# Kernel optimization log

Hardware: AMD Instinct MI355X
Metric: run time of the kernel (lower is better)

## Reference

```python
import jax, jax.numpy as jnp
import numpy as np

V = 100000   # input_size == output_size (item vocab)
H = 256      # hidden_size
B = 512      # batch_size
L = 1        # num_layers


def setup_inputs() -> dict:
    key = jax.random.key(0)
    k0, k1, k2, k3, k4 = jax.random.split(key, 5)
    s = 1.0 / np.sqrt(H)  # pytorch default uniform bound scale
    return {
        "input": jax.random.randint(k0, (B,), 0, V),
        "target": jax.random.randint(k1, (B,), 0, V),
        "hidden": jnp.zeros((L, B, H), jnp.float32),
        # GRU weights, pytorch gate layout [r; z; n]
        "w_ih": jax.random.uniform(k2, (3 * H, V), jnp.float32, -s, s),
        "w_hh": jax.random.uniform(k3, (3 * H, H), jnp.float32, -s, s),
        "b_ih": jnp.zeros((3 * H,), jnp.float32),
        "b_hh": jnp.zeros((3 * H,), jnp.float32),
        # h2o linear
        "w_out": jax.random.uniform(k4, (V, H), jnp.float32, -s, s),
        "b_out": jnp.zeros((V,), jnp.float32),
    }


def reference(input, target, hidden, w_ih, w_hh, b_ih, b_hh, w_out, b_out):
    # one-hot(input) @ w_ih.T is mathematically a column gather of w_ih
    h = hidden[0]                                        # (B, H)
    gi = jnp.take(w_ih, input, axis=1).T + b_ih          # (B, 3H)
    gh = h @ w_hh.T + b_hh                               # (B, 3H)
    i_r, i_z, i_n = jnp.split(gi, 3, axis=1)
    h_r, h_z, h_n = jnp.split(gh, 3, axis=1)
    r = jax.nn.sigmoid(i_r + h_r)
    z = jax.nn.sigmoid(i_z + h_z)
    n = jnp.tanh(i_n + r * h_n)
    h_new = (1.0 - z) * n + z * h                        # (B, H)
    logit = jnp.tanh(h_new @ w_out.T + b_out)            # (B, V)
    return logit, h_new[None]                            # ((B,V), (L,B,H))
```

## Files before the change

kernel.cpp:

```cpp
#include <hip/hip_runtime.h>
#include <hip/hip_bf16.h>
#include <math.h>

#define V 100000
#define H 256
#define B 512

typedef __bf16 bf16x8 __attribute__((ext_vector_type(8)));
typedef unsigned short u16x8 __attribute__((ext_vector_type(8)));
typedef float  f32x4  __attribute__((ext_vector_type(4)));

__device__ __forceinline__ unsigned short f32_bf16_rne(float x) {
    unsigned u = __float_as_uint(x);
    u += 0x7FFFu + ((u >> 16) & 1u);
    return (unsigned short)(u >> 16);
}
__device__ __forceinline__ float bf16u_f32(unsigned short h) {
    return __uint_as_float(((unsigned)h) << 16);
}
__device__ __forceinline__ float fast_tanh(float x) {
    float e = __builtin_exp2f(x * 2.8853900817779268f);
    return 1.f - 2.f * __builtin_amdgcn_rcpf(e + 1.f);
}

#define GLOAD_LDS16(g, l)                                                     \
    __builtin_amdgcn_global_load_lds(                                         \
        (const __attribute__((address_space(1))) void*)(g),                   \
        (__attribute__((address_space(3))) void*)(l), 16, 0, 0)

__global__ __launch_bounds__(256) void gru_cell_v3(
    const int*   __restrict__ input,
    const float* __restrict__ hidden,
    const float* __restrict__ w_ih,
    const float* __restrict__ w_hh,
    const float* __restrict__ b_ih,
    const float* __restrict__ b_hh,
    float*       __restrict__ h_out,
    unsigned short* __restrict__ h_hi_p,
    unsigned short* __restrict__ h_lo_p)
{
    const int gb  = blockIdx.x >> 2;
    const int q   = blockIdx.x & 3;
    const int b0  = gb * 8;
    const int j0  = q * 64;
    const int tid = threadIdx.x;
    const int jj  = tid & 63;
    const int bq  = tid >> 6;
    const int j   = j0 + jj;

    __shared__ float hs[8 * H];
    __shared__ int   idxs[8];
    #pragma unroll
    for (int i = 0; i < 2; ++i) {
        const int p = i * 256 + tid;
        reinterpret_cast<float4*>(hs)[p] =
            reinterpret_cast<const float4*>(hidden + (size_t)b0 * H)[p];
    }
    if (tid < 8) idxs[tid] = input[b0 + tid];
    __syncthreads();

    const int ba = bq * 2, bb = bq * 2 + 1;
    const int ia = idxs[ba], ib = idxs[bb];

    const float g_ra = w_ih[(size_t) j          * V + ia];
    const float g_rb = w_ih[(size_t) j          * V + ib];
    const float g_za = w_ih[(size_t)(j +     H) * V + ia];
    const float g_zb = w_ih[(size_t)(j +     H) * V + ib];
    const float g_na = w_ih[(size_t)(j + 2 * H) * V + ia];
    const float g_nb = w_ih[(size_t)(j + 2 * H) * V + ib];

    const float4* wr = reinterpret_cast<const float4*>(&w_hh[(size_t) j          * H]);
    const float4* wz = reinterpret_cast<const float4*>(&w_hh[(size_t)(j +     H) * H]);
    const float4* wn = reinterpret_cast<const float4*>(&w_hh[(size_t)(j + 2 * H) * H]);
    const float4* ha = reinterpret_cast<const float4*>(&hs[ba * H]);
    const float4* hb = reinterpret_cast<const float4*>(&hs[bb * H]);

    float ara = 0.f, aza = 0.f, ana = 0.f;
    float arb = 0.f, azb = 0.f, anb = 0.f;
    #pragma unroll 4
    for (int k = 0; k < H / 4; ++k) {
        const float4 a = wr[k];
        const float4 c = wz[k];
        const float4 d = wn[k];
        const float4 va = ha[k];
        const float4 vb = hb[k];
        ara += a.x * va.x + a.y * va.y + a.z * va.z + a.w * va.w;
        aza += c.x * va.x + c.y * va.y + c.z * va.z + c.w * va.w;
        ana += d.x * va.x + d.y * va.y + d.z * va.z + d.w * va.w;
        arb += a.x * vb.x + a.y * vb.y + a.z * vb.z + a.w * vb.w;
        azb += c.x * vb.x + c.y * vb.y + c.z * vb.z + c.w * vb.w;
        anb += d.x * vb.x + d.y * vb.y + d.z * vb.z + d.w * vb.w;
    }

    const float bir = b_ih[j], biz = b_ih[j + H], bin = b_ih[j + 2 * H];
    const float bhr = b_hh[j], bhz = b_hh[j + H], bhn = b_hh[j + 2 * H];

    #pragma unroll
    for (int s = 0; s < 2; ++s) {
        const float gi_r = (s ? g_rb : g_ra) + bir;
        const float gi_z = (s ? g_zb : g_za) + biz;
        const float gi_n = (s ? g_nb : g_na) + bin;
        const float h_r  = (s ? arb : ara) + bhr;
        const float h_z  = (s ? azb : aza) + bhz;
        const float h_n  = (s ? anb : ana) + bhn;
        const int   bg   = b0 + (s ? bb : ba);

        const float r = 1.f / (1.f + expf(-(gi_r + h_r)));
        const float z = 1.f / (1.f + expf(-(gi_z + h_z)));
        const float n = tanhf(gi_n + r * h_n);
        const float hprev = hs[(s ? bb : ba) * H + jj + j0];
        const float val = (1.f - z) * n + z * hprev;

        h_out[(size_t)bg * H + j] = val;
        if (h_hi_p != nullptr) {
            const unsigned short hh = f32_bf16_rne(val);
            h_hi_p[(size_t)bg * H + j] = hh;
            h_lo_p[(size_t)bg * H + j] = f32_bf16_rne(val - bf16u_f32(hh));
        }
    }
}

#define DBM  64
#define DBN  256
#define NVB3 391

__global__ __launch_bounds__(256, 2) void out_gemm_direct(
    const float*          __restrict__ w_out,
    const unsigned short* __restrict__ hhi_g,
    const unsigned short* __restrict__ hlo_g,
    const float*          __restrict__ b_out,
    float*                __restrict__ logit)
{
    __shared__ unsigned short h_hi_s[DBM * H];
    __shared__ unsigned short h_lo_s[DBM * H];

    const int tid  = threadIdx.x;
    const int lane = tid & 63;
    const int wid  = tid >> 6;

    const int bid = blockIdx.x;
    const int wg  = (bid & 7) * NVB3 + (bid >> 3);
    const int vb  = wg >> 3;
    const int bx  = wg & 7;
    const int b0  = bx * DBM;
    const int v0  = vb * DBN;
    const int vw  = v0 + wid * 64;

    #pragma unroll
    for (int i = 0; i < 8; ++i) {
        const int pbase = i * 4096 + (wid << 10);
        const int p     = pbase + (lane << 4);
        const int row   = p >> 9;
        const int kb    = p & 511;
        const int swz   = kb ^ ((row & 7) << 4);
        const size_t gb = (size_t)(b0 + row) * 512 + swz;
        GLOAD_LDS16((const char*)hhi_g + gb, (char*)h_hi_s + pbase);
        GLOAD_LDS16((const char*)hlo_g + gb, (char*)h_lo_s + pbase);
    }
    __syncthreads();

    f32x4 acc[4][4];
    #pragma unroll
    for (int m = 0; m < 4; ++m)
        #pragma unroll
        for (int n = 0; n < 4; ++n)
            acc[m][n] = f32x4{0.f, 0.f, 0.f, 0.f};

    auto loadW = [&](float4* wreg, int t) {
        #pragma unroll
        for (int n = 0; n < 4; ++n) {
            int v = vw + n * 16 + (lane & 15);
            if (v > V - 1) v = V - 1;
            const size_t bo = (size_t)v * 1024 + t * 128 + ((lane >> 4) << 5);
            wreg[n * 2]     = *reinterpret_cast<const float4*>(
                                  reinterpret_cast<const char*>(w_out) + bo);
            wreg[n * 2 + 1] = *reinterpret_cast<const float4*>(
                                  reinterpret_cast<const char*>(w_out) + bo + 16);
        }
    };

    auto step = [&](int t, const float4* wreg) {
        const int kbyte = t * 64 + ((lane >> 4) << 4);
        bf16x8 ah[4], al[4];
        #pragma unroll
        for (int m = 0; m < 4; ++m) {
            const int row = m * 16 + (lane & 15);
            const int off = row * 512 + (kbyte ^ ((row & 7) << 4));
            ah[m] = *reinterpret_cast<const bf16x8*>(
                        reinterpret_cast<const char*>(h_hi_s) + off);
            al[m] = *reinterpret_cast<const bf16x8*>(
                        reinterpret_cast<const char*>(h_lo_s) + off);
        }
        bf16x8 bh[4], bl[4];
        #pragma unroll
        for (int n = 0; n < 4; ++n) {
            const float4 fa = wreg[n * 2];
            const float4 fb = wreg[n * 2 + 1];
            const float f[8] = {fa.x, fa.y, fa.z, fa.w, fb.x, fb.y, fb.z, fb.w};
            u16x8 uh, ul;
            #pragma unroll
            for (int e = 0; e < 8; ++e) {
                const unsigned short hv = f32_bf16_rne(f[e]);
                uh[e] = hv;
                ul[e] = f32_bf16_rne(f[e] - bf16u_f32(hv));
            }
            bh[n] = __builtin_bit_cast(bf16x8, uh);
            bl[n] = __builtin_bit_cast(bf16x8, ul);
        }
        #pragma unroll
        for (int n = 0; n < 4; ++n) {
            #pragma unroll
            for (int m = 0; m < 4; ++m) {
                acc[m][n] = __builtin_amdgcn_mfma_f32_16x16x32_bf16(ah[m], bh[n], acc[m][n], 0, 0, 0);
                acc[m][n] = __builtin_amdgcn_mfma_f32_16x16x32_bf16(ah[m], bl[n], acc[m][n], 0, 0, 0);
                acc[m][n] = __builtin_amdgcn_mfma_f32_16x16x32_bf16(al[m], bh[n], acc[m][n], 0, 0, 0);
            }
        }
    };

    float4 wA[8], wB[8];
    loadW(wA, 0);
    #pragma unroll
    for (int tt = 0; tt < 4; ++tt) {
        loadW(wB, tt * 2 + 1);
        step(tt * 2, wA);
        if (tt < 3) loadW(wA, tt * 2 + 2);
        step(tt * 2 + 1, wB);
    }

    float bias[4];
    int   cols[4];
    #pragma unroll
    for (int n = 0; n < 4; ++n) {
        const int c = vw + n * 16 + (lane & 15);
        cols[n] = c;
        bias[n] = (c < V) ? b_out[c] : 0.f;
    }
    const int rbase = b0 + ((lane >> 4) << 2);
    #pragma unroll
    for (int m = 0; m < 4; ++m) {
        #pragma unroll
        for (int r = 0; r < 4; ++r) {
            const int row = rbase + m * 16 + r;
            float* dst = logit + (size_t)row * V;
            #pragma unroll
            for (int n = 0; n < 4; ++n) {
                if (cols[n] < V)
                    dst[cols[n]] = fast_tanh(acc[m][n][r] + bias[n]);
            }
        }
    }
}

#define BM  64
#define BN  128
#define BK  64
#define NVB 782
#define NBB 8

__global__ __launch_bounds__(256) void out_gemm_mfma_reg(
    const float* __restrict__ hnew,
    const float* __restrict__ w_out,
    const float* __restrict__ b_out,
    float*       __restrict__ logit)
{
    __shared__ unsigned short w_hi[BN * BK];
    __shared__ unsigned short w_lo[BN * BK];
    __shared__ unsigned short h_hi[BM * BK];
    __shared__ unsigned short h_lo[BM * BK];

    const int tid  = threadIdx.x;
    const int lane = tid & 63;
    const int wid  = tid >> 6;
    const int wm   = wid >> 1;
    const int wn   = wid & 1;

    const int bid = blockIdx.x;
    const int wg  = (bid & 7) * NVB + (bid >> 3);
    const int bx  = wg & 7;
    const int by  = wg >> 3;
    const int b0  = bx * BM;
    const int v0  = by * BN;

    float4 wreg[8];
    float4 hreg[4];

    auto load_chunk = [&](int k0) {
        #pragma unroll
        for (int i = 0; i < 8; ++i) {
            const int idx4 = i * 256 + tid;
            const int row  = idx4 >> 4;
            const int k4   = (idx4 & 15) << 2;
            int vg = v0 + row; if (vg > V - 1) vg = V - 1;
            wreg[i] = *reinterpret_cast<const float4*>(&w_out[(size_t)vg * H + k0 + k4]);
        }
        #pragma unroll
        for (int i = 0; i < 4; ++i) {
            const int idx4 = i * 256 + tid;
            const int row  = idx4 >> 4;
            const int k4   = (idx4 & 15) << 2;
            hreg[i] = *reinterpret_cast<const float4*>(&hnew[(b0 + row) * H + k0 + k4]);
        }
    };

    auto store_chunk = [&]() {
        #pragma unroll
        for (int i = 0; i < 8; ++i) {
            const int idx4 = i * 256 + tid;
            const int row  = idx4 >> 4;
            const int k4   = (idx4 & 15) << 2;
            const int off  = row * (BK * 2) + ((k4 * 2) ^ ((row & 7) << 4));
            const float f[4] = {wreg[i].x, wreg[i].y, wreg[i].z, wreg[i].w};
            unsigned short hv[4], lv[4];
            #pragma unroll
            for (int jj = 0; jj < 4; ++jj) {
                hv[jj] = f32_bf16_rne(f[jj]);
                lv[jj] = f32_bf16_rne(f[jj] - bf16u_f32(hv[jj]));
            }
            *reinterpret_cast<ushort4*>(reinterpret_cast<char*>(w_hi) + off) =
                make_ushort4(hv[0], hv[1], hv[2], hv[3]);
            *reinterpret_cast<ushort4*>(reinterpret_cast<char*>(w_lo) + off) =
                make_ushort4(lv[0], lv[1], lv[2], lv[3]);
        }
        #pragma unroll
        for (int i = 0; i < 4; ++i) {
            const int idx4 = i * 256 + tid;
            const int row  = idx4 >> 4;
            const int k4   = (idx4 & 15) << 2;
            const int off  = row * (BK * 2) + ((k4 * 2) ^ ((row & 7) << 4));
            const float f[4] = {hreg[i].x, hreg[i].y, hreg[i].z, hreg[i].w};
            unsigned short hv[4], lv[4];
            #pragma unroll
            for (int jj = 0; jj < 4; ++jj) {
                hv[jj] = f32_bf16_rne(f[jj]);
                lv[jj] = f32_bf16_rne(f[jj] - bf16u_f32(hv[jj]));
            }
            *reinterpret_cast<ushort4*>(reinterpret_cast<char*>(h_hi) + off) =
                make_ushort4(hv[0], hv[1], hv[2], hv[3]);
            *reinterpret_cast<ushort4*>(reinterpret_cast<char*>(h_lo) + off) =
                make_ushort4(lv[0], lv[1], lv[2], lv[3]);
        }
    };

    f32x4 acc[2][4];
    #pragma unroll
    for (int i = 0; i < 2; ++i)
        #pragma unroll
        for (int n = 0; n < 4; ++n)
            acc[i][n] = f32x4{0.f, 0.f, 0.f, 0.f};

    auto compute = [&]() {
        #pragma unroll
        for (int ks = 0; ks < 2; ++ks) {
            const int kb = ks * 64 + (lane >> 4) * 16;
            bf16x8 ah[2], al[2];
            #pragma unroll
            for (int i = 0; i < 2; ++i) {
                const int row = wm * 32 + i * 16 + (lane & 15);
                const int off = row * (BK * 2) + (kb ^ ((row & 7) << 4));
                ah[i] = *reinterpret_cast<const bf16x8*>(
                            reinterpret_cast<const char*>(h_hi) + off);
                al[i] = *reinterpret_cast<const bf16x8*>(
                            reinterpret_cast<const char*>(h_lo) + off);
            }
            #pragma unroll
            for (int n = 0; n < 4; ++n) {
                const int row = wn * 64 + n * 16 + (lane & 15);
                const int off = row * (BK * 2) + (kb ^ ((row & 7) << 4));
                const bf16x8 bh = *reinterpret_cast<const bf16x8*>(
                            reinterpret_cast<const char*>(w_hi) + off);
                const bf16x8 bl = *reinterpret_cast<const bf16x8*>(
                            reinterpret_cast<const char*>(w_lo) + off);
                #pragma unroll
                for (int i = 0; i < 2; ++i) {
                    acc[i][n] = __builtin_amdgcn_mfma_f32_16x16x32_bf16(ah[i], bh, acc[i][n], 0, 0, 0);
                    acc[i][n] = __builtin_amdgcn_mfma_f32_16x16x32_bf16(ah[i], bl, acc[i][n], 0, 0, 0);
                    acc[i][n] = __builtin_amdgcn_mfma_f32_16x16x32_bf16(al[i], bh, acc[i][n], 0, 0, 0);
                }
            }
        }
    };

    load_chunk(0);
    store_chunk();
    __syncthreads();
    for (int t = 0; t < 4; ++t) {
        if (t < 3) load_chunk((t + 1) * BK);
        compute();
        __syncthreads();
        if (t < 3) { store_chunk(); __syncthreads(); }
    }

    float bias[4];
    int   cols[4];
    #pragma unroll
    for (int n = 0; n < 4; ++n) {
        const int c = v0 + wn * 64 + n * 16 + (lane & 15);
        cols[n] = c;
        bias[n] = (c < V) ? b_out[c] : 0.f;
    }
    const int rbase = b0 + wm * 32 + (lane >> 4) * 4;
    #pragma unroll
    for (int i = 0; i < 2; ++i) {
        #pragma unroll
        for (int r = 0; r < 4; ++r) {
            const int row = rbase + i * 16 + r;
            float* dst = logit + (size_t)row * V;
            #pragma unroll
            for (int n = 0; n < 4; ++n) {
                if (cols[n] < V)
                    dst[cols[n]] = tanhf(acc[i][n][r] + bias[n]);
            }
        }
    }
}

extern "C" void kernel_launch(void* const* d_in, const int* in_sizes, int n_in,
                              void* d_out, int out_size, void* d_ws, size_t ws_size,
                              hipStream_t stream) {
    const int*   input  = (const int*)  d_in[0];
    const float* hidden = (const float*)d_in[2];
    const float* w_ih   = (const float*)d_in[3];
    const float* w_hh   = (const float*)d_in[4];
    const float* b_ih   = (const float*)d_in[5];
    const float* b_hh   = (const float*)d_in[6];
    const float* w_out  = (const float*)d_in[7];
    const float* b_out  = (const float*)d_in[8];

    float* out   = (float*)d_out;
    float* logit = out;
    float* h_new = out + (size_t)B * V;

    const size_t nh = (size_t)B * H;
    const size_t needed = 2 * nh * sizeof(unsigned short);

    if (ws_size >= needed) {
        unsigned short* hhi = (unsigned short*)d_ws;
        unsigned short* hlo = hhi + nh;

        gru_cell_v3<<<256, 256, 0, stream>>>(input, hidden, w_ih, w_hh,
                                             b_ih, b_hh, h_new, hhi, hlo);
        out_gemm_direct<<<NVB3 * 8, 256, 0, stream>>>(w_out, hhi, hlo,
                                                      b_out, logit);
    } else {
        gru_cell_v3<<<256, 256, 0, stream>>>(input, hidden, w_ih, w_hh,
                                             b_ih, b_hh, h_new,
                                             nullptr, nullptr);
        out_gemm_mfma_reg<<<NVB * NBB, 256, 0, stream>>>(h_new, w_out,
                                                         b_out, logit);
    }
}
```

Before: 257.5 us.

## Pre-split w_out into bf16 hi/lo planes in the GRU kernel, stage via LDS

Extra blocks in the GRU launch convert w_out from fp32 into bf16 hi and lo arrays in the workspace, running alongside the GRU cell work. The output GEMM then streams those pre-split bf16 tiles into LDS with direct global-to-LDS loads and takes the A operand from global memory, so the per-tile fp32-to-bf16 split inside the GEMM goes away. The cost is an extra full pass that reads w_out (about 100 MB) and writes about 100 MB of split planes, which the GEMM then reads back. It also needs a much larger workspace, and the GEMM uses smaller tiles with two barriers per K step.

New measurement: 239.5 us. 1.08x faster.

```diff
diff --git a/kernel.cpp b/kernel.cpp
--- a/kernel.cpp
+++ b/kernel.cpp
@@ -7,7 +7,6 @@
 #define B 512
 
 typedef __bf16 bf16x8 __attribute__((ext_vector_type(8)));
-typedef unsigned short u16x8 __attribute__((ext_vector_type(8)));
 typedef float  f32x4  __attribute__((ext_vector_type(4)));
 
 __device__ __forceinline__ unsigned short f32_bf16_rne(float x) {
@@ -28,17 +27,42 @@
         (const __attribute__((address_space(1))) void*)(g),                   \
         (__attribute__((address_space(3))) void*)(l), 16, 0, 0)
 
-__global__ __launch_bounds__(256) void gru_cell_v3(
+#define PREP_GRID 2304
+
+__global__ __launch_bounds__(256) void gru_and_split(
     const int*   __restrict__ input,
     const float* __restrict__ hidden,
     const float* __restrict__ w_ih,
     const float* __restrict__ w_hh,
     const float* __restrict__ b_ih,
     const float* __restrict__ b_hh,
+    const float* __restrict__ w_out,
     float*       __restrict__ h_out,
     unsigned short* __restrict__ h_hi_p,
-    unsigned short* __restrict__ h_lo_p)
+    unsigned short* __restrict__ h_lo_p,
+    unsigned short* __restrict__ w_hi_p,
+    unsigned short* __restrict__ w_lo_p)
 {
+    if (blockIdx.x >= 256) {
+        const int total4 = (V * H) / 4;
+        for (int i = (blockIdx.x - 256) * 256 + threadIdx.x; i < total4;
+             i += 2048 * 256) {
+            const float4 x = reinterpret_cast<const float4*>(w_out)[i];
+            const float f[4] = {x.x, x.y, x.z, x.w};
+            ushort4 hv, lv;
+            unsigned short* hp = &hv.x;
+            unsigned short* lp = &lv.x;
+            #pragma unroll
+            for (int jj = 0; jj < 4; ++jj) {
+                hp[jj] = f32_bf16_rne(f[jj]);
+                lp[jj] = f32_bf16_rne(f[jj] - bf16u_f32(hp[jj]));
+            }
+            reinterpret_cast<ushort4*>(w_hi_p)[i] = hv;
+            reinterpret_cast<ushort4*>(w_lo_p)[i] = lv;
+        }
+        return;
+    }
+
     const int gb  = blockIdx.x >> 2;
     const int q   = blockIdx.x & 3;
     const int b0  = gb * 8;
@@ -120,143 +144,134 @@
     }
 }
 
-#define DBM  64
-#define DBN  256
-#define NVB3 391
-
-__global__ __launch_bounds__(256, 2) void out_gemm_direct(
-    const float*          __restrict__ w_out,
+#define BM  64
+#define BN  128
+#define BK  64
+#define NVB 782
+#define NBB 8
+
+__global__ __launch_bounds__(256, 4) void out_gemm_lean(
+    const unsigned short* __restrict__ whi_g,
+    const unsigned short* __restrict__ wlo_g,
     const unsigned short* __restrict__ hhi_g,
     const unsigned short* __restrict__ hlo_g,
     const float*          __restrict__ b_out,
     float*                __restrict__ logit)
 {
-    __shared__ unsigned short h_hi_s[DBM * H];
-    __shared__ unsigned short h_lo_s[DBM * H];
+    __shared__ unsigned short w_hi_s[BN * BK];
+    __shared__ unsigned short w_lo_s[BN * BK];
 
     const int tid  = threadIdx.x;
     const int lane = tid & 63;
     const int wid  = tid >> 6;
+    const int wm   = wid >> 1;
+    const int wn   = wid & 1;
 
     const int bid = blockIdx.x;
-    const int wg  = (bid & 7) * NVB3 + (bid >> 3);
-    const int vb  = wg >> 3;
+    const int wg  = (bid & 7) * NVB + (bid >> 3);
     const int bx  = wg & 7;
-    const int b0  = bx * DBM;
-    const int v0  = vb * DBN;
-    const int vw  = v0 + wid * 64;
-
-    #pragma unroll
-    for (int i = 0; i < 8; ++i) {
-        const int pbase = i * 4096 + (wid << 10);
-        const int p     = pbase + (lane << 4);
-        const int row   = p >> 9;
-        const int kb    = p & 511;
-        const int swz   = kb ^ ((row & 7) << 4);
-        const size_t gb = (size_t)(b0 + row) * 512 + swz;
-        GLOAD_LDS16((const char*)hhi_g + gb, (char*)h_hi_s + pbase);
-        GLOAD_LDS16((const char*)hlo_g + gb, (char*)h_lo_s + pbase);
-    }
-    __syncthreads();
-
-    f32x4 acc[4][4];
-    #pragma unroll
-    for (int m = 0; m < 4; ++m)
+    const int by  = wg >> 3;
+    const int b0  = bx * BM;
+    const int v0  = by * BN;
+
+    auto stage = [&](int k0) {
+        #pragma unroll
+        for (int i = 0; i < 4; ++i) {
+            const int p    = i * 4096 + (wid << 10) + (lane << 4);
+            const int row  = p >> 7;
+            const int lb   = p & 127;
+            const int swz  = lb ^ ((row & 7) << 4);
+            int vg = v0 + row; if (vg > V - 1) vg = V - 1;
+            const size_t gb = (size_t)vg * (H * 2) + (size_t)(k0 * 2) + swz;
+            const int dst  = i * 4096 + (wid << 10);
+            GLOAD_LDS16((const char*)whi_g + gb, (char*)w_hi_s + dst);
+            GLOAD_LDS16((const char*)wlo_g + gb, (char*)w_lo_s + dst);
+        }
+    };
+
+    bf16x8 ah[4], al[4];
+    auto loadA = [&](int t) {
+        #pragma unroll
+        for (int i = 0; i < 2; ++i) {
+            #pragma unroll
+            for (int ks = 0; ks < 2; ++ks) {
+                const size_t ho = ((size_t)(b0 + wm * 32 + i * 16 + (lane & 15)) * H
+                                   + t * BK + ks * 32 + (lane >> 4) * 8) * 2;
+                ah[i * 2 + ks] = *reinterpret_cast<const bf16x8*>(
+                                     reinterpret_cast<const char*>(hhi_g) + ho);
+                al[i * 2 + ks] = *reinterpret_cast<const bf16x8*>(
+                                     reinterpret_cast<const char*>(hlo_g) + ho);
+            }
+        }
+    };
+
+    f32x4 acc[2][4];
+    #pragma unroll
+    for (int i = 0; i < 2; ++i)
         #pragma unroll
         for (int n = 0; n < 4; ++n)
-            acc[m][n] = f32x4{0.f, 0.f, 0.f, 0.f};
-
-    auto loadW = [&](float4* wreg, int t) {
-        #pragma unroll
-        for (int n = 0; n < 4; ++n) {
-            int v = vw + n * 16 + (lane & 15);
-            if (v > V - 1) v = V - 1;
-            const size_t bo = (size_t)v * 1024 + t * 128 + ((lane >> 4) << 5);
-            wreg[n * 2]     = *reinterpret_cast<const float4*>(
-                                  reinterpret_cast<const char*>(w_out) + bo);
-            wreg[n * 2 + 1] = *reinterpret_cast<const float4*>(
-                                  reinterpret_cast<const char*>(w_out) + bo + 16);
-        }
-    };
-
-    auto step = [&](int t, const float4* wreg) {
-        const int kbyte = t * 64 + ((lane >> 4) << 4);
-        bf16x8 ah[4], al[4];
-        #pragma unroll
-        for (int m = 0; m < 4; ++m) {
-            const int row = m * 16 + (lane & 15);
-            const int off = row * 512 + (kbyte ^ ((row & 7) << 4));
-            ah[m] = *reinterpret_cast<const bf16x8*>(
-                        reinterpret_cast<const char*>(h_hi_s) + off);
-            al[m] = *reinterpret_cast<const bf16x8*>(
-                        reinterpret_cast<const char*>(h_lo_s) + off);
-        }
-        bf16x8 bh[4], bl[4];
-        #pragma unroll
-        for (int n = 0; n < 4; ++n) {
-            const float4 fa = wreg[n * 2];
-            const float4 fb = wreg[n * 2 + 1];
-            const float f[8] = {fa.x, fa.y, fa.z, fa.w, fb.x, fb.y, fb.z, fb.w};
-            u16x8 uh, ul;
-            #pragma unroll
-            for (int e = 0; e < 8; ++e) {
-                const unsigned short hv = f32_bf16_rne(f[e]);
-                uh[e] = hv;
-                ul[e] = f32_bf16_rne(f[e] - bf16u_f32(hv));
-            }
-            bh[n] = __builtin_bit_cast(bf16x8, uh);
-            bl[n] = __builtin_bit_cast(bf16x8, ul);
-        }
-        #pragma unroll
-        for (int n = 0; n < 4; ++n) {
-            #pragma unroll
-            for (int m = 0; m < 4; ++m) {
-                acc[m][n] = __builtin_amdgcn_mfma_f32_16x16x32_bf16(ah[m], bh[n], acc[m][n], 0, 0, 0);
-                acc[m][n] = __builtin_amdgcn_mfma_f32_16x16x32_bf16(ah[m], bl[n], acc[m][n], 0, 0, 0);
-                acc[m][n] = __builtin_amdgcn_mfma_f32_16x16x32_bf16(al[m], bh[n], acc[m][n], 0, 0, 0);
-            }
-        }
-    };
-
-    float4 wA[8], wB[8];
-    loadW(wA, 0);
-    #pragma unroll
-    for (int tt = 0; tt < 4; ++tt) {
-        loadW(wB, tt * 2 + 1);
-        step(tt * 2, wA);
-        if (tt < 3) loadW(wA, tt * 2 + 2);
-        step(tt * 2 + 1, wB);
+            acc[i][n] = f32x4{0.f, 0.f, 0.f, 0.f};
+
+    auto compute = [&]() {
+        #pragma unroll
+        for (int ks = 0; ks < 2; ++ks) {
+            const int kb = ks * 64 + (lane >> 4) * 16;
+            bf16x8 bh[4], bl[4];
+            #pragma unroll
+            for (int n = 0; n < 4; ++n) {
+                const int row = wn * 64 + n * 16 + (lane & 15);
+                const int off = row * (BK * 2) + (kb ^ ((row & 7) << 4));
+                bh[n] = *reinterpret_cast<const bf16x8*>(
+                            reinterpret_cast<const char*>(w_hi_s) + off);
+                bl[n] = *reinterpret_cast<const bf16x8*>(
+                            reinterpret_cast<const char*>(w_lo_s) + off);
+            }
+            #pragma unroll
+            for (int n = 0; n < 4; ++n) {
+                #pragma unroll
+                for (int i = 0; i < 2; ++i) {
+                    const bf16x8 a_h = ah[i * 2 + ks];
+                    const bf16x8 a_l = al[i * 2 + ks];
+                    acc[i][n] = __builtin_amdgcn_mfma_f32_16x16x32_bf16(a_h, bh[n], acc[i][n], 0, 0, 0);
+                    acc[i][n] = __builtin_amdgcn_mfma_f32_16x16x32_bf16(a_h, bl[n], acc[i][n], 0, 0, 0);
+                    acc[i][n] = __builtin_amdgcn_mfma_f32_16x16x32_bf16(a_l, bh[n], acc[i][n], 0, 0, 0);
+                }
+            }
+        }
+    };
+
+    #pragma unroll
+    for (int t = 0; t < 4; ++t) {
+        stage(t * BK);
+        loadA(t);
+        __syncthreads();
+        compute();
+        __syncthreads();
     }
 
     float bias[4];
     int   cols[4];
     #pragma unroll
     for (int n = 0; n < 4; ++n) {
-        const int c = vw + n * 16 + (lane & 15);
+        const int c = v0 + wn * 64 + n * 16 + (lane & 15);
         cols[n] = c;
         bias[n] = (c < V) ? b_out[c] : 0.f;
     }
-    const int rbase = b0 + ((lane >> 4) << 2);
-    #pragma unroll
-    for (int m = 0; m < 4; ++m) {
+    const int rbase = b0 + wm * 32 + (lane >> 4) * 4;
+    #pragma unroll
+    for (int i = 0; i < 2; ++i) {
         #pragma unroll
         for (int r = 0; r < 4; ++r) {
-            const int row = rbase + m * 16 + r;
+            const int row = rbase + i * 16 + r;
             float* dst = logit + (size_t)row * V;
             #pragma unroll
             for (int n = 0; n < 4; ++n) {
                 if (cols[n] < V)
-                    dst[cols[n]] = fast_tanh(acc[m][n][r] + bias[n]);
-            }
-        }
-    }
-}
-
-#define BM  64
-#define BN  128
-#define BK  64
-#define NVB 782
-#define NBB 8
+                    dst[cols[n]] = fast_tanh(acc[i][n][r] + bias[n]);
+            }
+        }
+    }
+}
 
 __global__ __launch_bounds__(256) void out_gemm_mfma_reg(
     const float* __restrict__ hnew,
@@ -431,21 +446,25 @@
     float* logit = out;
     float* h_new = out + (size_t)B * V;
 
+    const size_t nw = (size_t)V * H;
     const size_t nh = (size_t)B * H;
-    const size_t needed = 2 * nh * sizeof(unsigned short);
+    const size_t needed = (2 * nw + 2 * nh) * sizeof(unsigned short);
 
     if (ws_size >= needed) {
-        unsigned short* hhi = (unsigned short*)d_ws;
+        unsigned short* whi = (unsigned short*)d_ws;
+        unsigned short* wlo = whi + nw;
+        unsigned short* hhi = wlo + nw;
         unsigned short* hlo = hhi + nh;
 
-        gru_cell_v3<<<256, 256, 0, stream>>>(input, hidden, w_ih, w_hh,
-                                             b_ih, b_hh, h_new, hhi, hlo);
-        out_gemm_direct<<<NVB3 * 8, 256, 0, stream>>>(w_out, hhi, hlo,
-                                                      b_out, logit);
+        gru_and_split<<<PREP_GRID, 256, 0, stream>>>(
+            input, hidden, w_ih, w_hh, b_ih, b_hh, w_out,
+            h_new, hhi, hlo, whi, wlo);
+        out_gemm_lean<<<NVB * NBB, 256, 0, stream>>>(whi, wlo, hhi, hlo,
+                                                     b_out, logit);
     } else {
-        gru_cell_v3<<<256, 256, 0, stream>>>(input, hidden, w_ih, w_hh,
-                                             b_ih, b_hh, h_new,
-                                             nullptr, nullptr);
+        gru_and_split<<<256, 256, 0, stream>>>(
+            input, hidden, w_ih, w_hh, b_ih, b_hh, w_out,
+            h_new, nullptr, nullptr, nullptr, nullptr);
         out_gemm_mfma_reg<<<NVB * NBB, 256, 0, stream>>>(h_new, w_out,
                                                          b_out, logit);
     }
```
